# Optimization experiments

Measured on AMD Instinct MI355X. Metric: run time of the kernel, lower is better.

The kernel has to match this reference:

```python
import jax, jax.numpy as jnp
import numpy as np

NEG_BIG = -9e15  # matches torch -9000000000000000.0

def setup_inputs() -> dict:
    key = jax.random.key(0)
    k1, k2, k3, k4 = jax.random.split(key, 4)
    B, N, F_IN, F_OUT = 8, 2048, 128, 64
    x = jax.random.normal(k1, (B, N, F_IN), dtype=jnp.float32)
    adj = jax.random.randint(k2, (B, N, N), 0, 2, dtype=jnp.int32)
    # xavier_uniform-style init for params
    limW = float(np.sqrt(6.0 / (F_IN + F_OUT)))
    W = jax.random.uniform(k3, (F_IN, F_OUT), minval=-limW, maxval=limW, dtype=jnp.float32)
    lima = float(np.sqrt(6.0 / (2 * F_OUT + 1)))
    a = jax.random.uniform(k4, (2 * F_OUT, 1), minval=-lima, maxval=lima, dtype=jnp.float32)
    return {"x": x, "adj": adj, "W": W, "a": a}

def reference(x, adj, W, a):
    # x: [B, N, F_in], adj: [B, N, N], W: [F_in, F_out], a: [2*F_out, 1]
    h = jnp.einsum('bnf,fo->bno', x, W)            # [B, N, F_out]
    F_out = W.shape[1]
    # The repeat/cat construction computes a_input[b,i,j] = [h_i ; h_j], so
    # a_input @ a decomposes into f1_i + f2_j without the O(N^2 * 2F) tensor.
    f1 = h @ a[:F_out, 0]                          # [B, N]
    f2 = h @ a[F_out:, 0]                          # [B, N]
    e = jnp.tanh(f1[:, :, None] + f2[:, None, :])  # [B, N, N]
    att = jnp.where(adj > 0, e, NEG_BIG)
    att = jax.nn.softmax(att, axis=2)              # [B, N, N]
    h_prime = jnp.einsum('bmn,bno->bmo', att, h)   # [B, N, F_out]
    return jax.nn.elu(h_prime)                     # concat=True branch
```

## Files before the change

kernel.cpp:

```cpp
#include <hip/hip_runtime.h>
#include <math.h>

#define BB 8
#define NN 2048
#define FIN 128
#define FOUT 64
#define TI 16
#define TJ 256
#define TJP (TJ + 8)
#define NTILE (NN / TJ)

typedef short bf16x8 __attribute__((ext_vector_type(8)));
typedef float f32x4 __attribute__((ext_vector_type(4)));

__device__ __forceinline__ float exp_tanh(float z) {
    float zc = fminf(fmaxf(z, -15.f), 15.f);
    float u = __expf(zc + zc);
    float tn = (u - 1.f) * __builtin_amdgcn_rcpf(u + 1.f);
    return __expf(tn);
}

__device__ __forceinline__ unsigned short f2bf(float x) {
    union { float f; unsigned u; } v; v.f = x;
    unsigned r = v.u + 0x7FFF + ((v.u >> 16) & 1);
    return (unsigned short)(r >> 16);
}

__global__ __launch_bounds__(256, 2) void gat_k1(const float* __restrict__ x,
                                                 const float* __restrict__ W,
                                                 const float* __restrict__ a,
                                                 unsigned short* __restrict__ ht,
                                                 float* __restrict__ f1,
                                                 float* __restrict__ f2) {
    __shared__ __attribute__((aligned(16))) float Wl[FIN][FOUT];
    __shared__ __attribute__((aligned(16))) float xs[16][FIN];
    int t = threadIdx.x;

    const float4* W4 = (const float4*)W;
    float4* Wl4 = (float4*)&Wl[0][0];
#pragma unroll
    for (int kk = 0; kk < 8; ++kk) Wl4[t + 256 * kk] = W4[t + 256 * kk];

    size_t row0 = (size_t)blockIdx.x * 16;
    const float4* x4 = (const float4*)(x + row0 * FIN);
    float4* xs4 = (float4*)&xs[0][0];
#pragma unroll
    for (int kk = 0; kk < 2; ++kk) xs4[t + 256 * kk] = x4[t + 256 * kk];
    __syncthreads();

    int c = t & 63;
    int rq = t >> 6;
    float acc[4] = {0.f, 0.f, 0.f, 0.f};
#pragma unroll 8
    for (int k = 0; k < FIN; ++k) {
        float wv = Wl[k][c];
        acc[0] = fmaf(xs[rq][k], wv, acc[0]);
        acc[1] = fmaf(xs[rq + 4][k], wv, acc[1]);
        acc[2] = fmaf(xs[rq + 8][k], wv, acc[2]);
        acc[3] = fmaf(xs[rq + 12][k], wv, acc[3]);
    }
    float a1c = a[c], a2c = a[FOUT + c];
#pragma unroll
    for (int m = 0; m < 4; ++m) {
        size_t bn = row0 + rq + 4 * m;
        int b = (int)(bn >> 11);
        int n = (int)(bn & 2047);
        ht[((size_t)b * FOUT + c) * NN + n] = f2bf(acc[m]);
        float p1 = acc[m] * a1c;
        float p2 = acc[m] * a2c;
#pragma unroll
        for (int off = 32; off > 0; off >>= 1) {
            p1 += __shfl_down(p1, off, 64);
            p2 += __shfl_down(p2, off, 64);
        }
        if (c == 0) { f1[bn] = p1; f2[bn] = p2; }
    }
}

__global__ __launch_bounds__(256) void gat_k2f(const int* __restrict__ adj,
                                               const unsigned short* __restrict__ ht,
                                               const float* __restrict__ f1,
                                               const float* __restrict__ f2,
                                               float* __restrict__ out) {
    __shared__ __attribute__((aligned(16))) unsigned short pb[TI][TJP];
    __shared__ __attribute__((aligned(16))) float f2s[TJ];
    __shared__ float f1s[TI];
    __shared__ float rsw[TI];

    int t = threadIdx.x;
    int i0 = blockIdx.x * TI;
    int b = blockIdx.y;

    int lane = t & 63;
    int w = t >> 6;
    int mrow = lane & 15;
    int quad = lane >> 4;

    int j4 = t & 63;

    if (t < TI) f1s[t] = f1[(size_t)b * NN + i0 + t];
    __syncthreads();

    float f1r[4];
    float ps[4];
#pragma unroll
    for (int m = 0; m < 4; ++m) {
        f1r[m] = f1s[w + 4 * m];
        ps[m] = 0.f;
    }
    f32x4 acc = {0.f, 0.f, 0.f, 0.f};

    const int* adjrow = adj + (((size_t)b * NN + i0) * NN) + 4 * j4;

    for (int jt = 0; jt < NTILE; ++jt) {
        int j0 = jt * TJ;

        int4 avreg[4];
#pragma unroll
        for (int m = 0; m < 4; ++m)
            avreg[m] = *(const int4*)(adjrow + (size_t)(w + 4 * m) * NN + j0);

        f2s[t] = f2[(size_t)b * NN + j0 + t];
        __syncthreads();

        float4 fv = ((const float4*)f2s)[j4];
#pragma unroll
        for (int m = 0; m < 4; ++m) {
            int4 av = avreg[m];
            float f1i = f1r[m];
            float4 p;
            p.x = (av.x > 0) ? exp_tanh(f1i + fv.x) : 0.f;
            p.y = (av.y > 0) ? exp_tanh(f1i + fv.y) : 0.f;
            p.z = (av.z > 0) ? exp_tanh(f1i + fv.z) : 0.f;
            p.w = (av.w > 0) ? exp_tanh(f1i + fv.w) : 0.f;
            ps[m] += p.x + p.y + p.z + p.w;
            ushort4 pk;
            pk.x = f2bf(p.x); pk.y = f2bf(p.y);
            pk.z = f2bf(p.z); pk.w = f2bf(p.w);
            *(ushort4*)&pb[w + 4 * m][4 * j4] = pk;
        }
        __syncthreads();

        const unsigned short* hp =
            ht + ((size_t)b * FOUT + w * 16 + mrow) * NN + j0 + 8 * quad;
        const unsigned short* prow = &pb[mrow][8 * quad];
#pragma unroll
        for (int ch = 0; ch < TJ / 32; ++ch) {
            bf16x8 af = *(const bf16x8*)(prow + 32 * ch);
            bf16x8 bf = *(const bf16x8*)(hp + 32 * ch);
            acc = __builtin_amdgcn_mfma_f32_16x16x32_bf16(af, bf, acc, 0, 0, 0);
        }
    }

#pragma unroll
    for (int m = 0; m < 4; ++m) {
        float s = ps[m];
#pragma unroll
        for (int off = 32; off > 0; off >>= 1) s += __shfl_down(s, off, 64);
        if (lane == 0) rsw[w + 4 * m] = s;
    }
    __syncthreads();

    float* op = out + ((size_t)b * NN + i0) * FOUT + w * 16 + mrow;
#pragma unroll
    for (int u = 0; u < 4; ++u) {
        int row = quad * 4 + u;
        float rinv = __builtin_amdgcn_rcpf(rsw[row]);
        float sx = acc[u] * rinv;
        op[(size_t)row * FOUT] = (sx > 0.f) ? sx : expm1f(sx);
    }
}

extern "C" void kernel_launch(void* const* d_in, const int* in_sizes, int n_in,
                              void* d_out, int out_size, void* d_ws, size_t ws_size,
                              hipStream_t stream) {
    const float* x   = (const float*)d_in[0];
    const int*   adj = (const int*)d_in[1];
    const float* W   = (const float*)d_in[2];
    const float* a   = (const float*)d_in[3];
    float* out = (float*)d_out;

    unsigned short* ht = (unsigned short*)d_ws;
    float* f1   = (float*)(ht + (size_t)BB * FOUT * NN);
    float* f2   = f1 + (size_t)BB * NN;

    gat_k1<<<dim3(BB * NN / 16), dim3(256), 0, stream>>>(x, W, a, ht, f1, f2);
    gat_k2f<<<dim3(NN / TI, BB), dim3(256), 0, stream>>>(adj, ht, f1, f2, out);
}
```

Baseline: 222.0 us.

## Restructure attention kernel to single-wave blocks with register double-buffered adjacency loads

Replaces the 256-thread, 16-row attention kernel with 64-thread single-wavefront blocks that each handle 8 rows. Adjacency and f2 tiles are prefetched into registers one tile ahead, and all __syncthreads barriers are removed. Each wave now computes all four 16-column output tiles with MFMA, using a 16-row P buffer whose upper 8 rows are zero padding. This wastes half of the MFMA work, re-reads h from global memory per row block, and raises register use for the 8x2 int4 prefetch buffers.

```diff
diff --git a/kernel.cpp b/kernel.cpp
--- a/kernel.cpp
+++ b/kernel.cpp
@@ -5,7 +5,7 @@
 #define NN 2048
 #define FIN 128
 #define FOUT 64
-#define TI 16
+#define TIW 8
 #define TJ 256
 #define TJP (TJ + 8)
 #define NTILE (NN / TJ)
@@ -77,97 +77,107 @@
     }
 }
 
-__global__ __launch_bounds__(256) void gat_k2f(const int* __restrict__ adj,
-                                               const unsigned short* __restrict__ ht,
-                                               const float* __restrict__ f1,
-                                               const float* __restrict__ f2,
-                                               float* __restrict__ out) {
-    __shared__ __attribute__((aligned(16))) unsigned short pb[TI][TJP];
-    __shared__ __attribute__((aligned(16))) float f2s[TJ];
-    __shared__ float f1s[TI];
-    __shared__ float rsw[TI];
-
-    int t = threadIdx.x;
-    int i0 = blockIdx.x * TI;
+__global__ __launch_bounds__(64) void gat_k2w(const int* __restrict__ adj,
+                                              const unsigned short* __restrict__ ht,
+                                              const float* __restrict__ f1,
+                                              const float* __restrict__ f2,
+                                              float* __restrict__ out) {
+    __shared__ __attribute__((aligned(16))) unsigned short pb[16][TJP];
+    int lane = threadIdx.x;
+    int i0 = blockIdx.x * TIW;
     int b = blockIdx.y;
 
-    int lane = t & 63;
-    int w = t >> 6;
     int mrow = lane & 15;
     int quad = lane >> 4;
 
-    int j4 = t & 63;
+    ushort4 z4 = {0, 0, 0, 0};
+#pragma unroll
+    for (int r = 8; r < 16; ++r) *(ushort4*)&pb[r][4 * lane] = z4;
 
-    if (t < TI) f1s[t] = f1[(size_t)b * NN + i0 + t];
-    __syncthreads();
+    float f1r[TIW];
+#pragma unroll
+    for (int r = 0; r < TIW; ++r) f1r[r] = f1[(size_t)b * NN + i0 + r];
 
-    float f1r[4];
-    float ps[4];
+    float ps[TIW];
 #pragma unroll
-    for (int m = 0; m < 4; ++m) {
-        f1r[m] = f1s[w + 4 * m];
-        ps[m] = 0.f;
-    }
-    f32x4 acc = {0.f, 0.f, 0.f, 0.f};
+    for (int r = 0; r < TIW; ++r) ps[r] = 0.f;
+    f32x4 acc[4];
+#pragma unroll
+    for (int ct = 0; ct < 4; ++ct) acc[ct] = (f32x4){0.f, 0.f, 0.f, 0.f};
 
-    const int* adjrow = adj + (((size_t)b * NN + i0) * NN) + 4 * j4;
+    const int* adjrow = adj + (((size_t)b * NN + i0) * NN) + 4 * lane;
+    const float* f2b = f2 + (size_t)b * NN + 4 * lane;
+    const unsigned short* htb = ht + (size_t)b * FOUT * NN;
 
+    int4 av[2][TIW];
+    float4 fv[2];
+#pragma unroll
+    for (int r = 0; r < TIW; ++r) av[0][r] = *(const int4*)(adjrow + (size_t)r * NN);
+    fv[0] = *(const float4*)f2b;
+
+#pragma unroll
     for (int jt = 0; jt < NTILE; ++jt) {
         int j0 = jt * TJ;
+        int cur = jt & 1;
 
-        int4 avreg[4];
+        if (jt + 1 < NTILE) {
 #pragma unroll
-        for (int m = 0; m < 4; ++m)
-            avreg[m] = *(const int4*)(adjrow + (size_t)(w + 4 * m) * NN + j0);
+            for (int r = 0; r < TIW; ++r)
+                av[cur ^ 1][r] = *(const int4*)(adjrow + (size_t)r * NN + j0 + TJ);
+            fv[cur ^ 1] = *(const float4*)(f2b + j0 + TJ);
+        }
 
-        f2s[t] = f2[(size_t)b * NN + j0 + t];
-        __syncthreads();
-
-        float4 fv = ((const float4*)f2s)[j4];
+        float4 f = fv[cur];
 #pragma unroll
-        for (int m = 0; m < 4; ++m) {
-            int4 av = avreg[m];
-            float f1i = f1r[m];
+        for (int r = 0; r < TIW; ++r) {
+            int4 a4 = av[cur][r];
+            float f1i = f1r[r];
             float4 p;
-            p.x = (av.x > 0) ? exp_tanh(f1i + fv.x) : 0.f;
-            p.y = (av.y > 0) ? exp_tanh(f1i + fv.y) : 0.f;
-            p.z = (av.z > 0) ? exp_tanh(f1i + fv.z) : 0.f;
-            p.w = (av.w > 0) ? exp_tanh(f1i + fv.w) : 0.f;
-            ps[m] += p.x + p.y + p.z + p.w;
+            p.x = (a4.x > 0) ? exp_tanh(f1i + f.x) : 0.f;
+            p.y = (a4.y > 0) ? exp_tanh(f1i + f.y) : 0.f;
+            p.z = (a4.z > 0) ? exp_tanh(f1i + f.z) : 0.f;
+            p.w = (a4.w > 0) ? exp_tanh(f1i + f.w) : 0.f;
+            ps[r] += p.x + p.y + p.z + p.w;
             ushort4 pk;
             pk.x = f2bf(p.x); pk.y = f2bf(p.y);
             pk.z = f2bf(p.z); pk.w = f2bf(p.w);
-            *(ushort4*)&pb[w + 4 * m][4 * j4] = pk;
+            *(ushort4*)&pb[r][4 * lane] = pk;
         }
-        __syncthreads();
 
-        const unsigned short* hp =
-            ht + ((size_t)b * FOUT + w * 16 + mrow) * NN + j0 + 8 * quad;
         const unsigned short* prow = &pb[mrow][8 * quad];
 #pragma unroll
         for (int ch = 0; ch < TJ / 32; ++ch) {
             bf16x8 af = *(const bf16x8*)(prow + 32 * ch);
-            bf16x8 bf = *(const bf16x8*)(hp + 32 * ch);
-            acc = __builtin_amdgcn_mfma_f32_16x16x32_bf16(af, bf, acc, 0, 0, 0);
+#pragma unroll
+            for (int ct = 0; ct < 4; ++ct) {
+                bf16x8 bf = *(const bf16x8*)(
+                    htb + (size_t)(ct * 16 + mrow) * NN + j0 + 8 * quad + 32 * ch);
+                acc[ct] = __builtin_amdgcn_mfma_f32_16x16x32_bf16(af, bf, acc[ct], 0, 0, 0);
+            }
         }
     }
 
+    float rsw[TIW];
 #pragma unroll
-    for (int m = 0; m < 4; ++m) {
-        float s = ps[m];
+    for (int r = 0; r < TIW; ++r) {
+        float s = ps[r];
 #pragma unroll
         for (int off = 32; off > 0; off >>= 1) s += __shfl_down(s, off, 64);
-        if (lane == 0) rsw[w + 4 * m] = s;
+        rsw[r] = __shfl(s, 0, 64);
     }
-    __syncthreads();
 
-    float* op = out + ((size_t)b * NN + i0) * FOUT + w * 16 + mrow;
 #pragma unroll
     for (int u = 0; u < 4; ++u) {
         int row = quad * 4 + u;
-        float rinv = __builtin_amdgcn_rcpf(rsw[row]);
-        float sx = acc[u] * rinv;
-        op[(size_t)row * FOUT] = (sx > 0.f) ? sx : expm1f(sx);
+        if (row < TIW) {
+            float rinv = __builtin_amdgcn_rcpf(rsw[row]);
+            float* op = out + ((size_t)b * NN + i0 + row) * FOUT + mrow;
+#pragma unroll
+            for (int ct = 0; ct < 4; ++ct) {
+                float sx = acc[ct][u] * rinv;
+                op[ct * 16] = (sx > 0.f) ? sx : expm1f(sx);
+            }
+        }
     }
 }
 
@@ -185,5 +195,5 @@
     float* f2   = f1 + (size_t)BB * NN;
 
     gat_k1<<<dim3(BB * NN / 16), dim3(256), 0, stream>>>(x, W, a, ht, f1, f2);
-    gat_k2f<<<dim3(NN / TI, BB), dim3(256), 0, stream>>>(adj, ht, f1, f2, out);
+    gat_k2w<<<dim3(NN / TIW, BB), dim3(64), 0, stream>>>(adj, ht, f1, f2, out);
 }
```

Result: slower. 296.8 us (+33.7%).
